# Optimization experiments

Measured on AMD Instinct MI355X. Metric: run time of the kernel, lower is better.

The kernel has to match this reference:

```python
import jax, jax.numpy as jnp
import numpy as np
import math

EPS = 1e-6
KP = -1.0  # Poincare ball curvature (c=1 -> kappa=-1)
KS = 1.0   # stereographic sphere projection (c=1 -> kappa=+1)

def _n(x):
    return jnp.sqrt(jnp.sum(x * x, -1, keepdims=True) + 1e-15)

def tan_k(u, k):
    if k < 0:
        return jnp.tanh(u)
    return jnp.tan(jnp.clip(u, -1.47079, 1.47079))

def artan_k(u, k):
    if k < 0:
        return jnp.arctanh(jnp.clip(u, -1 + 1e-5, 1 - 1e-5))
    return jnp.arctan(u)

def proj(x, k):
    if k < 0:
        n = _n(x)
        m = 1.0 - 1e-4
        return jnp.where(n > m, x * (m / n), x)
    return x

def expmap0(u, k):
    n = _n(u)
    return proj(tan_k(n, k) * u / n, k)

def logmap0(y, k):
    n = _n(y)
    return artan_k(n, k) * y / n

def _safe_den(d):
    return jnp.where(d >= 0, jnp.maximum(d, EPS), jnp.minimum(d, -EPS))

def mobius_add(x, y, k):
    x2 = jnp.sum(x * x, -1, keepdims=True)
    y2 = jnp.sum(y * y, -1, keepdims=True)
    xy = jnp.sum(x * y, -1, keepdims=True)
    num = (1 - 2 * k * xy - k * y2) * x + (1 + k * x2) * y
    den = 1 - 2 * k * xy + k * k * x2 * y2
    return proj(num / _safe_den(den), k)

def mobius_pw_mul(w, x, k):
    wx = w * x
    nx = _n(x)
    nwx = _n(wx)
    return proj(tan_k(nwx / nx * artan_k(nx, k), k) * wx / nwx, k)

def mobius_smul(r, x, k):
    n = _n(x)
    return proj(tan_k(r * artan_k(n, k), k) * x / n, k)

def wmid(xs, k, axis, w=None):
    lam = 2.0 / (1.0 + k * jnp.sum(xs * xs, -1, keepdims=True))
    if w is None:
        w = jnp.ones_like(lam)
    num = jnp.sum(w * lam * xs, axis=axis)
    den = jnp.abs(jnp.sum(w * (lam - 1.0), axis=axis))
    return mobius_smul(0.5, num / jnp.maximum(den, EPS), k)

def slin(x, W, b, k=None):
    if k is None:
        return x @ W.T + b
    return expmap0(logmap0(x, k) @ W.T + b, k)

def dist(x, y, k):
    return 2.0 * artan_k(_n(mobius_add(-x, y, k))[..., 0], k)

def hyp_attn(kk, q, v, k):
    # kk, v: [N,K,h]; q: [N,h]
    sc = -dist(q[:, None, :], kk, k)              # [N,K]
    a = jax.nn.softmax(sc, axis=1)[..., None]
    return wmid(v, k, axis=1, w=a)

def euc_attn(kk, q, v):
    sc = jnp.einsum('nkh,nh->nk', kk, q) / math.sqrt(kk.shape[-1])
    a = jax.nn.softmax(sc, axis=1)
    return jnp.einsum('nk,nkh->nh', a, v)


def _forward(x, h1, c1, h2, c2, h3, c3, del_t, iou1, iou2, iou3,
             Wq_w, Wq_b, Wc_w, Wc_b, Uf_w, Uf_b, Up_w, Up_b,
             Uiou_w, Uiou_b, d, nbr):
    sg, th = jax.nn.sigmoid, jnp.tanh
    # mailbox gather (message_func + DGL mailbox), [N,K,h]
    mh1, mh2, mh3 = h1[nbr], h2[nbr], h3[nbr]
    mc1, mc2, mc3 = c1[nbr], c2[nbr], c3[nbr]
    g_t = (d / (del_t[nbr] + 1.0))[..., None]      # [N,K,1]

    x_1p = slin(expmap0(x, KP), Wq_w, Wq_b, KP)
    x_1s = slin(expmap0(x, KS), Wq_w, Wq_b, KS)
    x_1e = slin(x, Wq_w, Wq_b)

    s1 = logmap0(sg(slin(mh1, Up_w, Up_b, KP)), KP)
    s2 = logmap0(sg(slin(mh2, Up_w, Up_b, KS)), KS)
    s3 = sg(slin(mh3, Up_w, Up_b))

    ht1p = mobius_pw_mul(s1, mh1, KP)
    ht2p = mobius_pw_mul(s2, expmap0(logmap0(mh2, KS), KP), KP)
    ht3p = mobius_pw_mul(s3, expmap0(mh3, KP), KP)
    h_1p = 3.0 * wmid(jnp.stack([ht1p, ht2p, ht3p]), KP, axis=0)

    ht1s = mobius_pw_mul(s1, expmap0(logmap0(mh1, KP), KS), KP)
    ht2s = mobius_pw_mul(s2, mh2, KS)
    ht3s = mobius_pw_mul(s3, expmap0(mh3, KS), KS)
    h_1s = 3.0 * wmid(jnp.stack([ht1s, ht2s, ht3s]), KP, axis=0)

    ht1e = logmap0(mobius_pw_mul(s1, mh1, KP), KP)
    ht2e = logmap0(mobius_pw_mul(s2, mh2, KS), KS)
    h_1e = ht1e + ht2e + s3 * mh3

    h_tildp = hyp_attn(h_1p, x_1p, h_1p, KP)
    h_tilds = hyp_attn(h_1s, x_1s, h_1s, KS)
    h_tilde = euc_attn(h_1e, x_1e, h_1e)

    # Poincare cell path
    csk_p = expmap0(th(logmap0(slin(mc1, Wc_w, Wc_b, KP), KP)), KP)
    ckt_p = mobius_add(mobius_add(-csk_p, mc1, KP), mobius_pw_mul(csk_p, g_t, KP), KP)
    f_p = sg(logmap0(slin(mh1, Uf_w, Uf_b, KP), KP))
    c_1 = wmid(mobius_pw_mul(f_p, ckt_p, KP), KP, axis=1)

    # Sphere cell path
    csk_s = expmap0(th(logmap0(slin(mc2, Wc_w, Wc_b, KS), KS)), KS)
    ckt_s = mobius_add(mobius_add(-csk_s, mc2, KS), mobius_pw_mul(csk_s, g_t, KS), KS)
    f_s = sg(logmap0(slin(mh2, Uf_w, Uf_b, KS), KS))
    c_2 = wmid(mobius_pw_mul(f_s, ckt_s, KS), KS, axis=1)

    # Euclidean cell path
    csk_e = th(slin(mc3, Wc_w, Wc_b))
    ckt_e = mc3 - csk_e + csk_e * g_t
    f_e = sg(slin(mh3, Uf_w, Uf_b))
    c_3 = jnp.sum(f_e * ckt_e, 1)

    niou1 = mobius_add(iou1, slin(h_tildp, Uiou_w, Uiou_b, KP), KP)
    niou2 = mobius_add(iou2, slin(h_tilds, Uiou_w, Uiou_b, KS), KS)
    niou3 = iou3 + slin(h_tilde, Uiou_w, Uiou_b)

    # apply_node_func
    i_p, o_p, u_p = jnp.split(niou1, 3, axis=1)
    i_p, o_p, u_p = sg(logmap0(i_p, KP)), sg(logmap0(o_p, KP)), th(logmap0(u_p, KP))
    i_s, o_s, u_s = jnp.split(niou2, 3, axis=1)
    i_s, o_s, u_s = sg(logmap0(i_s, KS)), sg(logmap0(o_s, KS)), th(logmap0(u_s, KS))
    i_e, o_e, u_e = jnp.split(niou3, 3, axis=1)
    i_e, o_e, u_e = sg(i_e), sg(o_e), th(u_e)

    nc1 = mobius_add(mobius_pw_mul(i_p, u_p, KP), c_1, KP)
    nc2 = mobius_add(mobius_pw_mul(i_s, u_s, KS), c_2, KS)
    nc3 = i_e * u_e + c_3
    nh1 = mobius_pw_mul(o_p, th(logmap0(nc1, KP)), KP)
    nh2 = mobius_pw_mul(o_s, th(logmap0(nc2, KS)), KS)
    nh3 = o_e * th(nc3)
    return jnp.stack([nh1, nc1, nh2, nc2, nh3, nc3])  # [6,N,h]


def setup_inputs() -> dict:
    N, K, H, X = 8192, 8, 128, 128
    key = jax.random.key(0)
    ks = jax.random.split(key, 24)
    def rn(i, shape, sc=0.05):
        return sc * jax.random.normal(ks[i], shape, jnp.float32)
    return dict(
        x=rn(0, (N, X)), h1=rn(1, (N, H)), c1=rn(2, (N, H)),
        h2=rn(3, (N, H)), c2=rn(4, (N, H)), h3=rn(5, (N, H)), c3=rn(6, (N, H)),
        del_t=jax.random.uniform(ks[7], (N,), jnp.float32),
        iou1=rn(8, (N, 3 * H)), iou2=rn(9, (N, 3 * H)), iou3=rn(10, (N, 3 * H)),
        Wq_w=rn(11, (H, X)), Wq_b=rn(12, (H,), 0.01),
        Wc_w=rn(13, (H, H)), Wc_b=rn(14, (H,), 0.01),
        Uf_w=rn(15, (H, H)), Uf_b=rn(16, (H,), 0.01),
        Up_w=rn(17, (H, H)), Up_b=rn(18, (H,), 0.01),
        Uiou_w=rn(19, (3 * H, H)), Uiou_b=rn(20, (3 * H,), 0.01),
        d=jnp.asarray(60.0, jnp.float32),
        nbr=jax.random.randint(ks[21], (N, K), 0, N),
    )


def reference(x, h1, c1, h2, c2, h3, c3, del_t, iou1, iou2, iou3,
              Wq_w, Wq_b, Wc_w, Wc_b, Uf_w, Uf_b, Up_w, Up_b,
              Uiou_w, Uiou_b, d, nbr):
    return _forward(x, h1, c1, h2, c2, h3, c3, del_t, iou1, iou2, iou3,
                    Wq_w, Wq_b, Wc_w, Wc_b, Uf_w, Uf_b, Up_w, Up_b,
                    Uiou_w, Uiou_b, d, nbr)
```

## Files before the change

kernel.cpp:

```cpp
#include <hip/hip_runtime.h>
#include <math.h>

#define HD 128
#define NNODE 8192
#define KNBR 8
#define NHS ((size_t)NNODE*(size_t)HD)

#define EPSF 1e-6f
#define PMX 0.9999f
#define ATHC (1.0f-1e-5f)
#define TANC 1.47079f

typedef unsigned short u16;
typedef unsigned int u32;
typedef __attribute__((ext_vector_type(8))) short short8;
typedef __attribute__((ext_vector_type(4))) float f32x4;
typedef __attribute__((ext_vector_type(2))) float f32x2;

static __device__ __forceinline__ float frcp(float x){ return __builtin_amdgcn_rcpf(x); }
static __device__ __forceinline__ float fdiv(float a,float b){ return a*__builtin_amdgcn_rcpf(b); }
static __device__ __forceinline__ float fsqrt(float x){ return __builtin_amdgcn_sqrtf(x); }
static __device__ __forceinline__ float fexp(float x){ return __builtin_amdgcn_exp2f(x*1.4426950408889634f); }
static __device__ __forceinline__ float flog(float x){ return __builtin_amdgcn_logf(x)*0.6931471805599453f; }
static __device__ __forceinline__ float ftanh(float x){
  float ax = fabsf(x);
  float e = fexp(-2.0f*ax);
  float t = (1.0f-e)*frcp(1.0f+e);
  return copysignf(t,x);
}
static __device__ __forceinline__ float fatanh(float x){
  x = fminf(fmaxf(x,-ATHC),ATHC);
  return 0.5f*flog((1.0f+x)*frcp(1.0f-x));
}
static __device__ __forceinline__ float fatan(float x){
  float ax = fabsf(x);
  bool inv = ax > 1.0f;
  float t = inv ? frcp(ax) : ax;
  float t2 = t*t;
  float p = -0.0117212f;
  p = p*t2 + 0.05265332f;
  p = p*t2 - 0.11643287f;
  p = p*t2 + 0.19354346f;
  p = p*t2 - 0.33262347f;
  p = p*t2 + 0.99997726f;
  float r = t*p;
  r = inv ? 1.5707963267948966f - r : r;
  return copysignf(r,x);
}
static __device__ __forceinline__ float ftan(float x){
  x = fminf(fmaxf(x,-TANC),TANC);
  float r = x*0.15915494309189535f;
  float s = __builtin_amdgcn_sinf(r);
  float c = __builtin_amdgcn_cosf(r);
  return s*frcp(c);
}
static __device__ __forceinline__ float sigm(float x){ return frcp(1.0f+fexp(-x)); }
static __device__ __forceinline__ float safeden(float d){
  return d>=0.0f ? fmaxf(d,EPSF) : fminf(d,-EPSF);
}

static __device__ __forceinline__ float wred(float v){
#pragma unroll
  for(int m=32;m;m>>=1) v += __shfl_xor(v,m,64);
  return v;
}
static __device__ __forceinline__ float hred16(float v){
#pragma unroll
  for(int m=8;m;m>>=1) v += __shfl_xor(v,m,64);
  return v;
}

static __device__ __forceinline__ u16 f2bf(float f){
  u32 u = __float_as_uint(f);
  u32 r = u + 0x7fffu + ((u>>16)&1u);
  return (u16)(r>>16);
}
static __device__ __forceinline__ float bf2f(u16 h){
  return __uint_as_float(((u32)h)<<16);
}
static __device__ __forceinline__ void split2(float v, u16* hp, u16* lp){
  u16 h = f2bf(v);
  float r = v - bf2f(h);
  *hp = h; *lp = f2bf(r);
}
static __device__ __forceinline__ void split2x2(float v0, float v1, u16* hp, u16* lp){
  u16 h0 = f2bf(v0), h1 = f2bf(v1);
  float r0 = v0 - bf2f(h0), r1 = v1 - bf2f(h1);
  *(u32*)hp = (u32)h0 | ((u32)h1<<16);
  *(u32*)lp = (u32)f2bf(r0) | ((u32)f2bf(r1)<<16);
}

#define SCOFF (27*NHS)
#define WOFF  (27*NHS + 49152)
#define NW    114688

__global__ __launch_bounds__(256) void k_pre(
    const float* __restrict__ x, const float* __restrict__ h1,
    const float* __restrict__ h2, const float* __restrict__ c1,
    const float* __restrict__ c2, const float* __restrict__ h3,
    const float* __restrict__ c3,
    const float* __restrict__ Wq, const float* __restrict__ Wc,
    const float* __restrict__ Uf, const float* __restrict__ Up,
    const float* __restrict__ Uiou, float* __restrict__ ws)
{
  if(blockIdx.x >= 2048){
    u16* WH = (u16*)(ws + WOFF);
    u16* WL = WH + NW;
    int idx0 = ((blockIdx.x-2048)*256 + threadIdx.x)*4;
#pragma unroll
    for(int q=0;q<4;q+=2){
      int idx = idx0 + q;
      float v0, v1;
      if(idx < 16384)      { v0=Wq[idx]; v1=Wq[idx+1]; }
      else if(idx < 32768) { v0=Wc[idx-16384]; v1=Wc[idx-16383]; }
      else if(idx < 49152) { v0=Uf[idx-32768]; v1=Uf[idx-32767]; }
      else if(idx < 65536) { v0=Up[idx-49152]; v1=Up[idx-49151]; }
      else                 { v0=Uiou[idx-65536]; v1=Uiou[idx-65535]; }
      split2x2(v0, v1, &WH[idx], &WL[idx]);
    }
    return;
  }
  int row = blockIdx.x*4 + (threadIdx.x>>6);
  int l = threadIdx.x & 63;
  size_t i0 = (size_t)row*HD + 2*l;
#define LD2(p) (*(const f32x2*)&p[i0])
  f32x2 xv = LD2(x);
  f32x2 h1v = LD2(h1), h2v = LD2(h2), h3v = LD2(h3);
  f32x2 c1v = LD2(c1), c2v = LD2(c2), c3v = LD2(c3);
#undef LD2
  float xa=xv[0], xb=xv[1];
  float h1a=h1v[0], h1b=h1v[1];
  float h2a=h2v[0], h2b=h2v[1];
  float c1a=c1v[0], c1b=c1v[1];
  float c2a=c2v[0], c2b=c2v[1];
  float h3a=h3v[0], h3b=h3v[1];
  float c3a=c3v[0], c3b=c3v[1];
  float xsq = wred(xa*xa+xb*xb);
  float h1sq = wred(h1a*h1a+h1b*h1b);
  float h2sq = wred(h2a*h2a+h2b*h2b);
  float c1sq = wred(c1a*c1a+c1b*c1b);
  float c2sq = wred(c2a*c2a+c2b*c2b);
  size_t p0 = i0;
#define WRSPLIT(R, va, vb) { \
    u16* hp = (u16*)(ws + (size_t)(R)*NHS); u16* lp2 = hp + NHS; \
    split2x2(va, vb, &hp[p0], &lp2[p0]); }
  float nx = fsqrt(xsq+1e-15f);
  {
    float t = ftanh(nx);
    float f = fminf(t,PMX)*frcp(nx);
    float ny = fsqrt(f*f*xsq + 1e-15f);
    float g = fatanh(ny)*frcp(ny) * f;
    WRSPLIT(0, g*xa, g*xb)
  }
  {
    float t = ftan(nx);
    float f = t*frcp(nx);
    float ny = fsqrt(f*f*xsq + 1e-15f);
    float g = fatan(ny)*frcp(ny) * f;
    WRSPLIT(1, g*xa, g*xb)
  }
  WRSPLIT(2, xa, xb)
  { float n=fsqrt(h1sq+1e-15f); float g=fatanh(n)*frcp(n); WRSPLIT(3, g*h1a, g*h1b) }
  { float n=fsqrt(h2sq+1e-15f); float g=fatan(n)*frcp(n);  WRSPLIT(4, g*h2a, g*h2b) }
  WRSPLIT(5, h3a, h3b)
  { float n=fsqrt(c1sq+1e-15f); float g=fatanh(n)*frcp(n); WRSPLIT(6, g*c1a, g*c1b) }
  { float n=fsqrt(c2sq+1e-15f); float g=fatan(n)*frcp(n);  WRSPLIT(7, g*c2a, g*c2b) }
  WRSPLIT(8, c3a, c3b)
#undef WRSPLIT
}

enum { P_ID=0, P_EXP_P, P_EXP_S, P_SIG, P_TANH, P_SIG_LOG_P, P_SIG_LOG_S,
       P_LOGSIG_P, P_LOGSIG_S, P_TANH_EXP_P, P_TANH_EXP_S };

struct JobM { const u16* Ah; const u16* Al; const u16* Wh; const u16* Wl;
              const float* b; float* out; int pitch; int post; };
struct JobTabM { JobM j[12]; };

__global__ __launch_bounds__(512) void k_gemmM(JobTabM tab){
  JobM jb = tab.j[blockIdx.y];
  __shared__ u16 Wlds[2*8*4*64*8];
  const int tid = threadIdx.x;
  for(int c = tid; c < 4096; c += 512){
    int lane_ = c & 63;
    int kk    = (c>>6)&3;
    int t     = (c>>8)&7;
    int plane = (c>>11)&1;
    const u16* src = (plane ? jb.Wl : jb.Wh)
                   + (size_t)(t*16 + (lane_&15))*128 + (lane_>>4)*8 + kk*32;
    *(uint4*)&Wlds[(size_t)c*8] = *(const uint4*)src;
  }
  const int lane = tid & 63;
  const int wave = tid >> 6;
  const int nn = lane & 15, quad = lane >> 4;
  float bias[8];
#pragma unroll
  for(int t=0;t<8;t++) bias[t] = jb.b[t*16+nn];
  __syncthreads();
  {
    const int row0 = blockIdx.x*128 + wave*16;
    const u16* Ah = jb.Ah + (size_t)(row0+nn)*128 + quad*8;
    const u16* Al = jb.Al + (size_t)(row0+nn)*128 + quad*8;
    f32x4 acc[8];
#pragma unroll
    for(int t=0;t<8;t++) acc[t] = (f32x4){0.f,0.f,0.f,0.f};
#pragma unroll
    for(int kk=0;kk<4;kk++){
      short8 ah = *(const short8*)(Ah + kk*32);
      short8 al = *(const short8*)(Al + kk*32);
#pragma unroll
      for(int t=0;t<8;t++){
        short8 wh = *(const short8*)&Wlds[(((0*8 + t)*4 + kk)*64 + lane)*8];
        short8 wl = *(const short8*)&Wlds[(((1*8 + t)*4 + kk)*64 + lane)*8];
        acc[t] = __builtin_amdgcn_mfma_f32_16x16x32_bf16(ah, wh, acc[t], 0,0,0);
        acc[t] = __builtin_amdgcn_mfma_f32_16x16x32_bf16(al, wh, acc[t], 0,0,0);
        acc[t] = __builtin_amdgcn_mfma_f32_16x16x32_bf16(ah, wl, acc[t], 0,0,0);
      }
    }
#pragma unroll
    for(int r=0;r<4;r++){
      float v[8];
#pragma unroll
      for(int t=0;t<8;t++) v[t] = acc[t][r] + bias[t];
      float s2 = 0.f;
#pragma unroll
      for(int t=0;t<8;t++) s2 += v[t]*v[t];
      float nraw = hred16(s2);
      switch(jb.post){
        case P_ID: break;
        case P_EXP_P: {
          float n=fsqrt(nraw+1e-15f); float tt=ftanh(n); float f=fminf(tt,PMX)*frcp(n);
          for(int t=0;t<8;t++) v[t]*=f;
        } break;
        case P_EXP_S: {
          float n=fsqrt(nraw+1e-15f); float f=ftan(n)*frcp(n);
          for(int t=0;t<8;t++) v[t]*=f;
        } break;
        case P_SIG:
          for(int t=0;t<8;t++) v[t]=sigm(v[t]);
          break;
        case P_TANH:
          for(int t=0;t<8;t++) v[t]=ftanh(v[t]);
          break;
        case P_SIG_LOG_P: {
          float n=fsqrt(nraw+1e-15f); float tt=ftanh(n); float f=fminf(tt,PMX)*frcp(n);
          float z[8]; float zs=0.f;
          for(int t=0;t<8;t++){ z[t]=sigm(f*v[t]); zs+=z[t]*z[t]; }
          float zr=hred16(zs);
          float zn=fsqrt(zr+1e-15f);
          float g=fatanh(zn)*frcp(zn);
          for(int t=0;t<8;t++) v[t]=g*z[t];
        } break;
        case P_SIG_LOG_S: {
          float n=fsqrt(nraw+1e-15f); float f=ftan(n)*frcp(n);
          float z[8]; float zs=0.f;
          for(int t=0;t<8;t++){ z[t]=sigm(f*v[t]); zs+=z[t]*z[t]; }
          float zr=hred16(zs);
          float zn=fsqrt(zr+1e-15f);
          float g=fatan(zn)*frcp(zn);
          for(int t=0;t<8;t++) v[t]=g*z[t];
        } break;
        case P_LOGSIG_P: {
          float n=fsqrt(nraw+1e-15f); float tt=ftanh(n); float f=fminf(tt,PMX)*frcp(n);
          float ny=fsqrt(f*f*nraw+1e-15f);
          float g=fatanh(ny)*frcp(ny)*f;
          for(int t=0;t<8;t++) v[t]=sigm(g*v[t]);
        } break;
        case P_LOGSIG_S: {
          float n=fsqrt(nraw+1e-15f); float f=ftan(n)*frcp(n);
          float ny=fsqrt(f*f*nraw+1e-15f);
          float g=fatan(ny)*frcp(ny)*f;
          for(int t=0;t<8;t++) v[t]=sigm(g*v[t]);
        } break;
        case P_TANH_EXP_P: {
          float n=fsqrt(nraw+1e-15f); float tt=ftanh(n); float f=fminf(tt,PMX)*frcp(n);
          float ny=fsqrt(f*f*nraw+1e-15f);
          float g=fatanh(ny)*frcp(ny)*f;
          float T[8]; float Ts=0.f;
          for(int t=0;t<8;t++){ T[t]=ftanh(g*v[t]); Ts+=T[t]*T[t]; }
          float Tr=hred16(Ts);
          float Tn=fsqrt(Tr+1e-15f);
          float t2=ftanh(Tn); float f2=fminf(t2,PMX)*frcp(Tn);
          for(int t=0;t<8;t++) v[t]=f2*T[t];
        } break;
        case P_TANH_EXP_S: {
          float n=fsqrt(nraw+1e-15f); float f=ftan(n)*frcp(n);
          float ny=fsqrt(f*f*nraw+1e-15f);
          float g=fatan(ny)*frcp(ny)*f;
          float T[8]; float Ts=0.f;
          for(int t=0;t<8;t++){ T[t]=ftanh(g*v[t]); Ts+=T[t]*T[t]; }
          float Tr=hred16(Ts);
          float Tn=fsqrt(Tr+1e-15f);
          float f2=ftan(Tn)*frcp(Tn);
          for(int t=0;t<8;t++) v[t]=f2*T[t];
        } break;
      }
      float* orow = jb.out + (size_t)(row0 + quad*4 + r)*jb.pitch + nn;
#pragma unroll
      for(int t=0;t<8;t++) orow[t*16] = v[t];
    }
  }
}

__global__ __launch_bounds__(256) void k_phaseB(
  const float* __restrict__ h1,const float* __restrict__ h2,const float* __restrict__ h3,
  const float* __restrict__ c1,const float* __restrict__ c2,const float* __restrict__ c3,
  const float* __restrict__ del_t, const float* __restrict__ dsc,
  float* __restrict__ ws)
{
  const float* S1 = ws+9*NHS;  const float* S2 = ws+10*NHS; const float* S3 = ws+11*NHS;
  const float* F1 = ws+12*NHS; const float* F2 = ws+13*NHS; const float* F3 = ws+14*NHS;
  const float* Q1 = ws+15*NHS; const float* Q2 = ws+16*NHS; const float* Q3 = ws+17*NHS;
  f32x2* PKP = (f32x2*)(ws+21*NHS);
  f32x2* PKS = (f32x2*)(ws+22*NHS);
  f32x2* PKE = (f32x2*)(ws+23*NHS);
  f32x4* PKV4= (f32x4*)(ws+24*NHS);
  f32x2* PKV2= (f32x2*)(ws+26*NHS);
  f32x4* SC4 = (f32x4*)(ws+SCOFF);

  int j = blockIdx.x*4 + (threadIdx.x>>6);
  int l = threadIdx.x&63;
  size_t i0 = (size_t)j*HD + 2*l;
  size_t pix = (size_t)j*64 + l;
#define LD2(p) (*(const f32x2*)&p[i0])
  f32x2 h1v=LD2(h1), h2v=LD2(h2), h3v=LD2(h3);
  f32x2 c1v=LD2(c1), c2v=LD2(c2), c3v=LD2(c3);
  f32x2 s1v=LD2(S1), s2v=LD2(S2), s3v=LD2(S3);
  f32x2 f1v=LD2(F1), f2v=LD2(F2), f3v=LD2(F3);
  f32x2 q1v=LD2(Q1), q2v=LD2(Q2), q3v=LD2(Q3);
#undef LD2
  float h1a=h1v[0],h1b=h1v[1], h2a=h2v[0],h2b=h2v[1], h3a=h3v[0],h3b=h3v[1];
  float c1a=c1v[0],c1b=c1v[1], c2a=c2v[0],c2b=c2v[1], c3a=c3v[0],c3b=c3v[1];
  float s1a=s1v[0],s1b=s1v[1], s2a=s2v[0],s2b=s2v[1], s3a=s3v[0],s3b=s3v[1];
  float f1a=f1v[0],f1b=f1v[1], f2a=f2v[0],f2b=f2v[1], f3a=f3v[0],f3b=f3v[1];
  float q1a=q1v[0],q1b=q1v[1], q2a=q2v[0],q2b=q2v[1], q3a=q3v[0],q3b=q3v[1];
  float g = fdiv(dsc[0], del_t[j]+1.0f);

  float h1sq = wred(h1a*h1a+h1b*h1b); float n1 = fsqrt(h1sq+1e-15f);
  float h2sq = wred(h2a*h2a+h2b*h2b); float n2 = fsqrt(h2sq+1e-15f);
  float h3sq = wred(h3a*h3a+h3b*h3b); float n3 = fsqrt(h3sq+1e-15f);
  float w1a=s1a*h1a, w1b=s1b*h1b;
  float w2a=s2a*h2a, w2b=s2b*h2b;
  float w3a=s3a*h3a, w3b=s3b*h3b;
  float w1sq = wred(w1a*w1a+w1b*w1b); float nw1 = fsqrt(w1sq+1e-15f);
  float w2sq = wred(w2a*w2a+w2b*w2b); float nw2 = fsqrt(w2sq+1e-15f);
  float w3sq = wred(w3a*w3a+w3b*w3b); float nw3 = fsqrt(w3sq+1e-15f);

  float t1 = ftanh(nw1*frcp(n1) * fatanh(n1));
  float fp1 = fminf(t1,PMX)*frcp(nw1); float np1 = fminf(t1,PMX);
  float nu2 = fatan(n2);
  float ne2 = fminf(ftanh(nu2),PMX);
  float t2 = ftanh(nw2*frcp(n2) * fatanh(ne2));
  float fp2 = fminf(t2,PMX)*frcp(nw2); float np2 = fminf(t2,PMX);
  float ne3 = fminf(ftanh(n3),PMX);
  float t3 = ftanh(nw3*frcp(n3) * fatanh(ne3));
  float fp3 = fminf(t3,PMX)*frcp(nw3); float np3 = fminf(t3,PMX);
  float y2pv;
  {
    float lamA = 2.0f*frcp(1.0f-np1*np1), lamB = 2.0f*frcp(1.0f-np2*np2), lamC = 2.0f*frcp(1.0f-np3*np3);
    float dn = frcp(fmaxf(fabsf(lamA+lamB+lamC-3.0f), EPSF));
    float va = (lamA*fp1*w1a + lamB*fp2*w2a + lamC*fp3*w3a)*dn;
    float vb = (lamA*fp1*w1b + lamB*fp2*w2b + lamC*fp3*w3b)*dn;
    float vsq = wred(va*va+vb*vb); float nv = fsqrt(vsq+1e-15f);
    float tt = ftanh(0.5f*fatanh(nv)); float ff = 3.0f*fminf(tt,PMX)*frcp(nv);
    PKP[pix] = (f32x2){ff*va, ff*vb};
    y2pv = ff*ff*vsq;
  }
  float t2s, fs2, y2sv;
  {
    float nx1s = ftan(fatanh(n1));
    float t1s = ftanh(nw1*frcp(n1) * fatanh(nx1s));
    float fs1 = fminf(t1s,PMX)*frcp(nw1); float ns1 = fminf(t1s,PMX);
    t2s = ftan(nw2*frcp(n2) * fatan(n2));
    fs2 = t2s*frcp(nw2);
    float nx3s = ftan(n3);
    float t3s = ftan(nw3*frcp(n3) * fatan(nx3s));
    float fs3 = t3s*frcp(nw3);
    float lA = 2.0f*frcp(1.0f-ns1*ns1), lB = 2.0f*frcp(1.0f-t2s*t2s), lC = 2.0f*frcp(1.0f-t3s*t3s);
    float dns = frcp(fmaxf(fabsf(lA+lB+lC-3.0f), EPSF));
    float vsa = (lA*fs1*w1a + lB*fs2*w2a + lC*fs3*w3a)*dns;
    float vsb = (lA*fs1*w1b + lB*fs2*w2b + lC*fs3*w3b)*dns;
    float vssq = wred(vsa*vsa+vsb*vsb); float nvs = fsqrt(vssq+1e-15f);
    float tts = ftan(0.5f*fatan(nvs)); float ffs = 3.0f*tts*frcp(nvs);
    PKS[pix] = (f32x2){ffs*vsa, ffs*vsb};
    y2sv = ffs*ffs*vssq;
  }
  {
    float ne1 = fsqrt(fp1*fp1*w1sq + 1e-15f);
    float ge1 = fatanh(ne1)*frcp(ne1);
    float n2s_ = fsqrt(fs2*fs2*w2sq + 1e-15f);
    float ge2 = fatan(n2s_)*frcp(n2s_);
    float h1ea = ge1*fp1*w1a + ge2*fs2*w2a + s3a*h3a;
    float h1eb = ge1*fp1*w1b + ge2*fs2*w2b + s3b*h3b;
    PKE[pix] = (f32x2){h1ea, h1eb};
  }
  float ng = fsqrt(g*g+1e-15f);
  float v1xa,v1xb,d1v;
  {
    float q1sq = wred(q1a*q1a+q1b*q1b);
    float c1rs = wred(c1a*c1a+c1b*c1b);
    float dq1 = wred(q1a*c1a+q1b*c1b);
    float xy = -dq1;
    float aa = 1.0f+2.0f*xy+c1rs, bb = 1.0f-q1sq;
    float dd = frcp(safeden(1.0f+2.0f*xy+q1sq*c1rs));
    float m1a = (aa*(-q1a)+bb*c1a)*dd, m1b = (aa*(-q1b)+bb*c1b)*dd;
    float m1sq = (aa*aa*q1sq + 2.0f*aa*bb*xy + bb*bb*c1rs)*dd*dd;
    float mdq = (-aa*q1sq + bb*dq1)*dd;
    { float nm = fsqrt(m1sq+1e-15f);
      if(nm>PMX){ float sc=PMX*frcp(nm); m1a*=sc; m1b*=sc; m1sq*=sc*sc; mdq*=sc; } }
    float nwg = fsqrt(g*g*q1sq+1e-15f);
    float tg = ftanh(nwg*frcp(ng) * fatanh(ng));
    float fX = fminf(tg,PMX)*frcp(nwg) * g;
    float X2sq = fX*fX*q1sq;
    float xy2 = fX*mdq;
    float a2 = 1.0f+2.0f*xy2+X2sq, b2 = 1.0f-m1sq;
    float d2d = frcp(safeden(1.0f+2.0f*xy2+m1sq*X2sq));
    float ka = (a2*m1a + b2*fX*q1a)*d2d, kb = (a2*m1b + b2*fX*q1b)*d2d;
    float ksq = (a2*a2*m1sq + 2.0f*a2*b2*xy2 + b2*b2*X2sq)*d2d*d2d;
    { float nk0 = fsqrt(ksq+1e-15f);
      if(nk0>PMX){ float sc=PMX*frcp(nk0); ka*=sc; kb*=sc; ksq*=sc*sc; } }
    float nk = fsqrt(ksq+1e-15f);
    float wfa = f1a*ka, wfb = f1b*kb;
    float wfsq = wred(wfa*wfa+wfb*wfb); float nwf = fsqrt(wfsq+1e-15f);
    float tu = ftanh(nwf*frcp(nk) * fatanh(nk));
    float fu = fminf(tu,PMX)*frcp(nwf);
    float u1sq = fu*fu*wfsq;
    float lam = 2.0f*frcp(1.0f-u1sq);
    v1xa=lam*fu*wfa; v1xb=lam*fu*wfb;
    d1v=lam-1.0f;
  }
  float v2xa,v2xb,d2v;
  {
    float q2sq = wred(q2a*q2a+q2b*q2b);
    float c2rs = wred(c2a*c2a+c2b*c2b);
    float dq2 = wred(q2a*c2a+q2b*c2b);
    float xy = -dq2;
    float aa = 1.0f-2.0f*xy-c2rs, bb = 1.0f+q2sq;
    float dd = frcp(safeden(1.0f-2.0f*xy+q2sq*c2rs));
    float ma = (aa*(-q2a)+bb*c2a)*dd, mb = (aa*(-q2b)+bb*c2b)*dd;
    float msq = (aa*aa*q2sq + 2.0f*aa*bb*xy + bb*bb*c2rs)*dd*dd;
    float mdq = (-aa*q2sq + bb*dq2)*dd;
    float nwg = fsqrt(g*g*q2sq+1e-15f);
    float tg = ftan(nwg*frcp(ng) * fatan(ng));
    float fX = tg*frcp(nwg) * g;
    float X2sq = fX*fX*q2sq;
    float xy2 = fX*mdq;
    float a2 = 1.0f-2.0f*xy2-X2sq, b2 = 1.0f+msq;
    float d2d = frcp(safeden(1.0f-2.0f*xy2+msq*X2sq));
    float ka = (a2*ma + b2*fX*q2a)*d2d, kb = (a2*mb + b2*fX*q2b)*d2d;
    float ksq = (a2*a2*msq + 2.0f*a2*b2*xy2 + b2*b2*X2sq)*d2d*d2d;
    float nk = fsqrt(ksq+1e-15f);
    float wfa = f2a*ka, wfb = f2b*kb;
    float wfsq = wred(wfa*wfa+wfb*wfb); float nwf = fsqrt(wfsq+1e-15f);
    float tu = ftan(nwf*frcp(nk) * fatan(nk));
    float fu = tu*frcp(nwf);
    float u2sq = fu*fu*wfsq;
    float lam = 2.0f*frcp(1.0f+u2sq);
    v2xa=lam*fu*wfa; v2xb=lam*fu*wfb;
    d2v=lam-1.0f;
  }
  float v3xa,v3xb;
  {
    float kea = c3a + q3a*(g-1.0f), keb = c3b + q3b*(g-1.0f);
    v3xa=f3a*kea; v3xb=f3b*keb;
  }
  PKV4[pix] = (f32x4){v1xa,v1xb,v2xa,v2xb};
  PKV2[pix] = (f32x2){v3xa,v3xb};
  if(l==0) SC4[j] = (f32x4){y2pv,y2sv,d1v,d2v};
}

__global__ __launch_bounds__(256) void k_attn(
  const int* __restrict__ nbr, float* __restrict__ ws)
{
  const f32x2* PKP = (const f32x2*)(ws+21*NHS);
  const f32x2* PKS = (const f32x2*)(ws+22*NHS);
  const f32x2* PKE = (const f32x2*)(ws+23*NHS);
  const f32x4* PKV4= (const f32x4*)(ws+24*NHS);
  const f32x2* PKV2= (const f32x2*)(ws+26*NHS);
  const float* SCf = ws+SCOFF;
  u16* LPh = (u16*)(ws+9*NHS);  u16* LPl = LPh + NHS;
  u16* LSh = (u16*)(ws+10*NHS); u16* LSl = LSh + NHS;
  u16* LEh = (u16*)(ws+11*NHS); u16* LEl = LEh + NHS;
  float* C1o = ws+12*NHS; float* C2o = ws+13*NHS; float* C3o = ws+14*NHS;
  float* c1n2 = ws+SCOFF+32768; float* c2n2 = ws+SCOFF+40960;

  int n = blockIdx.x;
  int wv = threadIdx.x>>6;
  int l = threadIdx.x&63;
  size_t i0 = (size_t)n*HD + 2*l;
  int4 jA = ((const int4*)nbr)[n*2+0];
  int4 jB = ((const int4*)nbr)[n*2+1];
  int js[8] = {jA.x,jA.y,jA.z,jA.w,jB.x,jB.y,jB.z,jB.w};

  if(wv==0){
    const float* XP = ws+18*NHS;
    f32x2 xv = *(const f32x2*)&XP[i0];
    float XPa=xv[0], XPb=xv[1];
    float x2p = wred(XPa*XPa+XPb*XPb);
    float Ha[8],Hb[8],y2k[8];
#pragma unroll
    for(int k=0;k<8;k++){
      int j = js[k];
      f32x2 h = PKP[(size_t)j*64+l];
      Ha[k]=h[0]; Hb[k]=h[1];
      y2k[k]=SCf[(size_t)j*4+0];
    }
    float sc[8];
#pragma unroll
    for(int k=0;k<8;k++){
      float dp = wred(XPa*Ha[k]+XPb*Hb[k]);
      float xy=-dp, y2=y2k[k];
      float aa=1.0f+2.0f*xy+y2, bb=1.0f-x2p;
      float dd=frcp(safeden(1.0f+2.0f*xy+x2p*y2));
      float nsq=(aa*aa*x2p+2.0f*aa*bb*xy+bb*bb*y2)*dd*dd;
      float nn=fminf(fsqrt(nsq+1e-15f),PMX);
      sc[k] = -2.0f*fatanh(nn);
    }
    float mx=sc[0];
#pragma unroll
    for(int k=1;k<8;k++) mx=fmaxf(mx,sc[k]);
    float a[8]; float s=0;
#pragma unroll
    for(int k=0;k<8;k++){ a[k]=fexp(sc[k]-mx); s+=a[k]; }
    float inv=frcp(s);
    float na=0,nb=0,de=0;
#pragma unroll
    for(int k=0;k<8;k++){
      float lam = 2.0f*frcp(1.0f-y2k[k]); float w=a[k]*inv;
      na+=w*lam*Ha[k]; nb+=w*lam*Hb[k]; de+=w*(lam-1.0f);
    }
    de = frcp(fmaxf(fabsf(de),EPSF));
    na*=de; nb*=de;
    float vsq=wred(na*na+nb*nb); float nv=fsqrt(vsq+1e-15f);
    float tt=ftanh(0.5f*fatanh(nv)); float f=fminf(tt,PMX)*frcp(nv);
    float ha=f*na, hb=f*nb;
    float hn=fsqrt(f*f*vsq+1e-15f);
    float gl=fatanh(hn)*frcp(hn);
    split2x2(gl*ha, gl*hb, &LPh[i0], &LPl[i0]);
  } else if(wv==1){
    const float* XS = ws+19*NHS;
    f32x2 xv = *(const f32x2*)&XS[i0];
    float XSa=xv[0], XSb=xv[1];
    float x2s = wred(XSa*XSa+XSb*XSb);
    float Ha[8],Hb[8],y2k[8];
#pragma unroll
    for(int k=0;k<8;k++){
      int j = js[k];
      f32x2 h = PKS[(size_t)j*64+l];
      Ha[k]=h[0]; Hb[k]=h[1];
      y2k[k]=SCf[(size_t)j*4+1];
    }
    float sc[8];
#pragma unroll
    for(int k=0;k<8;k++){
      float dsv = wred(XSa*Ha[k]+XSb*Hb[k]);
      float xy=-dsv, y2=y2k[k];
      float aa=1.0f-2.0f*xy-y2, bb=1.0f+x2s;
      float dd=frcp(safeden(1.0f-2.0f*xy+x2s*y2));
      float nsq=(aa*aa*x2s+2.0f*aa*bb*xy+bb*bb*y2)*dd*dd;
      float nn=fsqrt(nsq+1e-15f);
      sc[k] = -2.0f*fatan(nn);
    }
    float mx=sc[0];
#pragma unroll
    for(int k=1;k<8;k++) mx=fmaxf(mx,sc[k]);
    float a[8]; float s=0;
#pragma unroll
    for(int k=0;k<8;k++){ a[k]=fexp(sc[k]-mx); s+=a[k]; }
    float inv=frcp(s);
    float na=0,nb=0,de=0;
#pragma unroll
    for(int k=0;k<8;k++){
      float lam = 2.0f*frcp(1.0f+y2k[k]); float w=a[k]*inv;
      na+=w*lam*Ha[k]; nb+=w*lam*Hb[k]; de+=w*(lam-1.0f);
    }
    de = frcp(fmaxf(fabsf(de),EPSF));
    na*=de; nb*=de;
    float vsq=wred(na*na+nb*nb); float nv=fsqrt(vsq+1e-15f);
    float tt=ftan(0.5f*fatan(nv)); float f=tt*frcp(nv);
    float ha=f*na, hb=f*nb;
    float hn=fsqrt(f*f*vsq+1e-15f);
    float gl=fatan(hn)*frcp(hn);
    split2x2(gl*ha, gl*hb, &LSh[i0], &LSl[i0]);
  } else if(wv==2){
    const float* XE = ws+20*NHS;
    const float rs = 0.08838834764831845f;
    f32x2 xv = *(const f32x2*)&XE[i0];
    float XEa=xv[0], XEb=xv[1];
    float Ha[8],Hb[8];
#pragma unroll
    for(int k=0;k<8;k++){
      int j = js[k];
      f32x2 h = PKE[(size_t)j*64+l];
      Ha[k]=h[0]; Hb[k]=h[1];
    }
    float sc[8];
#pragma unroll
    for(int k=0;k<8;k++) sc[k] = wred(XEa*Ha[k]+XEb*Hb[k])*rs;
    float mx=sc[0];
#pragma unroll
    for(int k=1;k<8;k++) mx=fmaxf(mx,sc[k]);
    float a[8]; float s=0;
#pragma unroll
    for(int k=0;k<8;k++){ a[k]=fexp(sc[k]-mx); s+=a[k]; }
    float inv=frcp(s);
    float ha=0,hb=0;
#pragma unroll
    for(int k=0;k<8;k++){ float w=a[k]*inv; ha+=w*Ha[k]; hb+=w*Hb[k]; }
    split2x2(ha, hb, &LEh[i0], &LEl[i0]);
  } else {
    float v1a=0,v1b=0,v2a=0,v2b=0,v3a=0,v3b=0,ds1=0,ds2=0;
#pragma unroll
    for(int k=0;k<8;k++){
      int j = js[k];
      f32x4 v4 = PKV4[(size_t)j*64+l];
      f32x2 v2 = PKV2[(size_t)j*64+l];
      v1a+=v4[0]; v1b+=v4[1]; v2a+=v4[2]; v2b+=v4[3];
      v3a+=v2[0]; v3b+=v2[1];
      ds1+=SCf[(size_t)j*4+2]; ds2+=SCf[(size_t)j*4+3];
    }
    {
      float de=frcp(fmaxf(fabsf(ds1),EPSF));
      float na=v1a*de, nb=v1b*de;
      float vsq=wred(na*na+nb*nb); float nv=fsqrt(vsq+1e-15f);
      float tt=ftanh(0.5f*fatanh(nv)); float f=fminf(tt,PMX)*frcp(nv);
      *(f32x2*)&C1o[i0] = (f32x2){f*na, f*nb};
      if(l==0) c1n2[n]=f*f*vsq;
    }
    {
      float de=frcp(fmaxf(fabsf(ds2),EPSF));
      float na=v2a*de, nb=v2b*de;
      float vsq=wred(na*na+nb*nb); float nv=fsqrt(vsq+1e-15f);
      float tt=ftan(0.5f*fatan(nv)); float f=tt*frcp(nv);
      *(f32x2*)&C2o[i0] = (f32x2){f*na, f*nb};
      if(l==0) c2n2[n]=f*f*vsq;
    }
    *(f32x2*)&C3o[i0] = (f32x2){v3a, v3b};
  }
}

__global__ __launch_bounds__(256) void k_final(
  const float* __restrict__ iou1, const float* __restrict__ iou2,
  const float* __restrict__ iou3, float* __restrict__ ws,
  float* __restrict__ out)
{
  const float* YP = ws; const float* YS = ws+3*NHS; const float* YE = ws+6*NHS;
  const float* C1v = ws+12*NHS; const float* C2v = ws+13*NHS; const float* C3v = ws+14*NHS;
  const float* c1n2 = ws+SCOFF+32768; const float* c2n2 = ws+SCOFF+40960;
  int n = blockIdx.x*4 + (threadIdx.x>>6);
  int l = threadIdx.x&63;
  size_t b384 = (size_t)n*384 + 2*l;
  size_t b128 = (size_t)n*HD + 2*l;
  {
    float Y[6], I[6];
#pragma unroll
    for(int p=0;p<3;p++){
      f32x2 yv = *(const f32x2*)&YP[b384 + 128*p];
      f32x2 iv = *(const f32x2*)&iou1[b384 + 128*p];
      Y[2*p]=yv[0]; Y[2*p+1]=yv[1]; I[2*p]=iv[0]; I[2*p+1]=iv[1];
    }
    float sy=0,si=0,sx=0;
#pragma unroll
    for(int r=0;r<6;r++){ sy+=Y[r]*Y[r]; si+=I[r]*I[r]; sx+=I[r]*Y[r]; }
    sy=wred(sy); si=wred(si); sx=wred(sx);
    float nY=fsqrt(sy+1e-15f);
    float te=ftanh(nY); float fE=fminf(te,PMX)*frcp(nY);
    float y2=fE*fE*sy, x2=si, xy=fE*sx;
    float aa=1.0f+2.0f*xy+y2, bb=1.0f-x2;
    float dd=frcp(safeden(1.0f+2.0f*xy+x2*y2));
    float nio[6];
#pragma unroll
    for(int r=0;r<6;r++) nio[r]=(aa*I[r]+bb*fE*Y[r])*dd;
    float nsq=(aa*aa*x2+2.0f*aa*bb*xy+bb*bb*y2)*dd*dd;
    { float nn=fsqrt(nsq+1e-15f);
      if(nn>PMX){ float sc=PMX*frcp(nn); for(int r=0;r<6;r++) nio[r]*=sc; } }
    float ci=wred(nio[0]*nio[0]+nio[1]*nio[1]); float ni=fsqrt(ci+1e-15f); float gi=fatanh(ni)*frcp(ni);
    float ip0=sigm(gi*nio[0]), ip1=sigm(gi*nio[1]);
    float co=wred(nio[2]*nio[2]+nio[3]*nio[3]); float no=fsqrt(co+1e-15f); float go=fatanh(no)*frcp(no);
    float op0=sigm(go*nio[2]), op1=sigm(go*nio[3]);
    float cu=wred(nio[4]*nio[4]+nio[5]*nio[5]); float nu=fsqrt(cu+1e-15f); float gu=fatanh(nu)*frcp(nu);
    float up0=ftanh(gu*nio[4]), up1=ftanh(gu*nio[5]);
    float usq=wred(up0*up0+up1*up1); float nx=fsqrt(usq+1e-15f);
    float wv0=ip0*up0, wv1=ip1*up1;
    float wsq=wred(wv0*wv0+wv1*wv1); float nwx=fsqrt(wsq+1e-15f);
    float tP=ftanh(nwx*frcp(nx)*fatanh(nx)); float fP=fminf(tP,PMX)*frcp(nwx);
    float P0=fP*wv0, P1=fP*wv1; float p2=fP*fP*wsq;
    f32x2 cv = *(const f32x2*)&C1v[b128];
    float ca=cv[0], cb=cv[1];
    float y2c=c1n2[n];
    float xyc=wred(P0*ca+P1*cb);
    float a3=1.0f+2.0f*xyc+y2c, b3=1.0f-p2;
    float d3=frcp(safeden(1.0f+2.0f*xyc+p2*y2c));
    float nc0=(a3*P0+b3*ca)*d3, nc1_=(a3*P1+b3*cb)*d3;
    float ncsq=(a3*a3*p2+2.0f*a3*b3*xyc+b3*b3*y2c)*d3*d3;
    { float nn=fsqrt(ncsq+1e-15f);
      if(nn>PMX){ float sc=PMX*frcp(nn); nc0*=sc; nc1_*=sc; ncsq*=sc*sc; } }
    float nl=fsqrt(ncsq+1e-15f);
    float gL=fatanh(nl)*frcp(nl);
    float T0=ftanh(gL*nc0), T1=ftanh(gL*nc1_);
    float tsq=wred(T0*T0+T1*T1); float nT=fsqrt(tsq+1e-15f);
    float wo0=op0*T0, wo1=op1*T1;
    float osq=wred(wo0*wo0+wo1*wo1); float nwo=fsqrt(osq+1e-15f);
    float tH=ftanh(nwo*frcp(nT)*fatanh(nT)); float fH=fminf(tH,PMX)*frcp(nwo);
    *(f32x2*)&out[0*NHS + b128] = (f32x2){fH*wo0, fH*wo1};
    *(f32x2*)&out[1*NHS + b128] = (f32x2){nc0, nc1_};
  }
  {
    float Y[6], I[6];
#pragma unroll
    for(int p=0;p<3;p++){
      f32x2 yv = *(const f32x2*)&YS[b384 + 128*p];
      f32x2 iv = *(const f32x2*)&iou2[b384 + 128*p];
      Y[2*p]=yv[0]; Y[2*p+1]=yv[1]; I[2*p]=iv[0]; I[2*p+1]=iv[1];
    }
    float sy=0,si=0,sx=0;
#pragma unroll
    for(int r=0;r<6;r++){ sy+=Y[r]*Y[r]; si+=I[r]*I[r]; sx+=I[r]*Y[r]; }
    sy=wred(sy); si=wred(si); sx=wred(sx);
    float nY=fsqrt(sy+1e-15f);
    float te=ftan(nY); float fE=te*frcp(nY);
    float y2=fE*fE*sy, x2=si, xy=fE*sx;
    float aa=1.0f-2.0f*xy-y2, bb=1.0f+x2;
    float dd=frcp(safeden(1.0f-2.0f*xy+x2*y2));
    float nio[6];
#pragma unroll
    for(int r=0;r<6;r++) nio[r]=(aa*I[r]+bb*fE*Y[r])*dd;
    float ci=wred(nio[0]*nio[0]+nio[1]*nio[1]); float ni=fsqrt(ci+1e-15f); float gi=fatan(ni)*frcp(ni);
    float ip0=sigm(gi*nio[0]), ip1=sigm(gi*nio[1]);
    float co=wred(nio[2]*nio[2]+nio[3]*nio[3]); float no=fsqrt(co+1e-15f); float go=fatan(no)*frcp(no);
    float op0=sigm(go*nio[2]), op1=sigm(go*nio[3]);
    float cu=wred(nio[4]*nio[4]+nio[5]*nio[5]); float nu=fsqrt(cu+1e-15f); float gu=fatan(nu)*frcp(nu);
    float up0=ftanh(gu*nio[4]), up1=ftanh(gu*nio[5]);
    float usq=wred(up0*up0+up1*up1); float nx=fsqrt(usq+1e-15f);
    float wv0=ip0*up0, wv1=ip1*up1;
    float wsq=wred(wv0*wv0+wv1*wv1); float nwx=fsqrt(wsq+1e-15f);
    float tP=ftan(nwx*frcp(nx)*fatan(nx)); float fP=tP*frcp(nwx);
    float P0=fP*wv0, P1=fP*wv1; float p2=fP*fP*wsq;
    f32x2 cv = *(const f32x2*)&C2v[b128];
    float ca=cv[0], cb=cv[1];
    float y2c=c2n2[n];
    float xyc=wred(P0*ca+P1*cb);
    float a3=1.0f-2.0f*xyc-y2c, b3=1.0f+p2;
    float d3=frcp(safeden(1.0f-2.0f*xyc+p2*y2c));
    float nc0=(a3*P0+b3*ca)*d3, nc1_=(a3*P1+b3*cb)*d3;
    float ncsq=(a3*a3*p2+2.0f*a3*b3*xyc+b3*b3*y2c)*d3*d3;
    float nl=fsqrt(ncsq+1e-15f);
    float gL=fatan(nl)*frcp(nl);
    float T0=ftanh(gL*nc0), T1=ftanh(gL*nc1_);
    float tsq=wred(T0*T0+T1*T1); float nT=fsqrt(tsq+1e-15f);
    float wo0=op0*T0, wo1=op1*T1;
    float osq=wred(wo0*wo0+wo1*wo1); float nwo=fsqrt(osq+1e-15f);
    float tH=ftan(nwo*frcp(nT)*fatan(nT)); float fH=tH*frcp(nwo);
    *(f32x2*)&out[2*NHS + b128] = (f32x2){fH*wo0, fH*wo1};
    *(f32x2*)&out[3*NHS + b128] = (f32x2){nc0, nc1_};
  }
  {
    float Y[6], I[6];
#pragma unroll
    for(int p=0;p<3;p++){
      f32x2 yv = *(const f32x2*)&YE[b384 + 128*p];
      f32x2 iv = *(const f32x2*)&iou3[b384 + 128*p];
      Y[2*p]=yv[0]; Y[2*p+1]=yv[1]; I[2*p]=iv[0]; I[2*p+1]=iv[1];
    }
    float n0=I[0]+Y[0], n1=I[1]+Y[1];
    float n2=I[2]+Y[2], n3=I[3]+Y[3];
    float n4=I[4]+Y[4], n5=I[5]+Y[5];
    float ie0=sigm(n0), ie1=sigm(n1);
    float oe0=sigm(n2), oe1=sigm(n3);
    float ue0=ftanh(n4), ue1=ftanh(n5);
    f32x2 cv = *(const f32x2*)&C3v[b128];
    float ca=cv[0], cb=cv[1];
    float nc0=ie0*ue0+ca, nc1_=ie1*ue1+cb;
    *(f32x2*)&out[4*NHS + b128] = (f32x2){oe0*ftanh(nc0), oe1*ftanh(nc1_)};
    *(f32x2*)&out[5*NHS + b128] = (f32x2){nc0, nc1_};
  }
}

extern "C" void kernel_launch(void* const* d_in, const int* in_sizes, int n_in,
                              void* d_out, int out_size, void* d_ws, size_t ws_size,
                              hipStream_t stream)
{
  const float* x     = (const float*)d_in[0];
  const float* h1    = (const float*)d_in[1];
  const float* c1    = (const float*)d_in[2];
  const float* h2    = (const float*)d_in[3];
  const float* c2    = (const float*)d_in[4];
  const float* h3    = (const float*)d_in[5];
  const float* c3    = (const float*)d_in[6];
  const float* del_t = (const float*)d_in[7];
  const float* iou1  = (const float*)d_in[8];
  const float* iou2  = (const float*)d_in[9];
  const float* iou3  = (const float*)d_in[10];
  const float* Wq_w  = (const float*)d_in[11];
  const float* Wq_b  = (const float*)d_in[12];
  const float* Wc_w  = (const float*)d_in[13];
  const float* Wc_b  = (const float*)d_in[14];
  const float* Uf_w  = (const float*)d_in[15];
  const float* Uf_b  = (const float*)d_in[16];
  const float* Up_w  = (const float*)d_in[17];
  const float* Up_b  = (const float*)d_in[18];
  const float* Uiou_w= (const float*)d_in[19];
  const float* Uiou_b= (const float*)d_in[20];
  const float* dsc   = (const float*)d_in[21];
  const int*   nbr   = (const int*)d_in[22];
  float* out = (float*)d_out;
  float* ws  = (float*)d_ws;

  k_pre<<<2160,256,0,stream>>>(x,h1,h2,c1,c2,h3,c3,Wq_w,Wc_w,Uf_w,Up_w,Uiou_w,ws);

  u16* WH = (u16*)(ws + WOFF);
  u16* WL = WH + NW;
  const u16* Wqh = WH;           const u16* Wql = WL;
  const u16* Wch = WH + 16384;   const u16* Wcl = WL + 16384;
  const u16* Ufh = WH + 32768;   const u16* Ufl = WL + 32768;
  const u16* Uph = WH + 49152;   const u16* Upl = WL + 49152;
  const u16* UIh = WH + 65536;   const u16* UIl = WL + 65536;
#define APLANE(R) ((const u16*)(ws + (size_t)(R)*NHS)), ((const u16*)(ws + (size_t)(R)*NHS) + NHS)

  JobTabM A{};
  A.j[0]  = { APLANE(0), Wqh, Wql, Wq_b, ws+18*NHS, 128, P_EXP_P };
  A.j[1]  = { APLANE(1), Wqh, Wql, Wq_b, ws+19*NHS, 128, P_EXP_S };
  A.j[2]  = { APLANE(2), Wqh, Wql, Wq_b, ws+20*NHS, 128, P_ID };
  A.j[3]  = { APLANE(3), Uph, Upl, Up_b, ws+9*NHS,  128, P_SIG_LOG_P };
  A.j[4]  = { APLANE(4), Uph, Upl, Up_b, ws+10*NHS, 128, P_SIG_LOG_S };
  A.j[5]  = { APLANE(5), Uph, Upl, Up_b, ws+11*NHS, 128, P_SIG };
  A.j[6]  = { APLANE(3), Ufh, Ufl, Uf_b, ws+12*NHS, 128, P_LOGSIG_P };
  A.j[7]  = { APLANE(4), Ufh, Ufl, Uf_b, ws+13*NHS, 128, P_LOGSIG_S };
  A.j[8]  = { APLANE(5), Ufh, Ufl, Uf_b, ws+14*NHS, 128, P_SIG };
  A.j[9]  = { APLANE(6), Wch, Wcl, Wc_b, ws+15*NHS, 128, P_TANH_EXP_P };
  A.j[10] = { APLANE(7), Wch, Wcl, Wc_b, ws+16*NHS, 128, P_TANH_EXP_S };
  A.j[11] = { APLANE(8), Wch, Wcl, Wc_b, ws+17*NHS, 128, P_TANH };
  k_gemmM<<<dim3(NNODE/128,12),512,0,stream>>>(A);

  k_phaseB<<<2048,256,0,stream>>>(h1,h2,h3,c1,c2,c3,del_t,dsc,ws);
  k_attn<<<8192,256,0,stream>>>(nbr,ws);

  JobTabM B{};
  for(int ct=0; ct<3; ct++){
    B.j[0*3+ct] = { APLANE(9),  UIh + ct*16384, UIl + ct*16384, Uiou_b + ct*128, ws+0*NHS + ct*128, 384, P_ID };
    B.j[1*3+ct] = { APLANE(10), UIh + ct*16384, UIl + ct*16384, Uiou_b + ct*128, ws+3*NHS + ct*128, 384, P_ID };
    B.j[2*3+ct] = { APLANE(11), UIh + ct*16384, UIl + ct*16384, Uiou_b + ct*128, ws+6*NHS + ct*128, 384, P_ID };
  }
  k_gemmM<<<dim3(NNODE/128,9),512,0,stream>>>(B);

  k_final<<<2048,256,0,stream>>>(iou1,iou2,iou3,ws,out);
}
```

Baseline: 258.5 us.

## Store intermediate workspace tensors in fp16 and prefetch GEMM A operands before LDS fill

All intermediate buffers passed between kernels (GEMM outputs, the packed neighbor keys and values in phaseB and attention, the attention outputs, and the second GEMM's iou outputs) are now stored as fp16 instead of fp32. Values are converted back to fp32 on load. This halves the memory traffic of the workspace reads and writes, including the random neighbor gathers in k_attn. The GEMM kernel also issues its A-operand global loads before the LDS weight fill, so those loads overlap the fill and the barrier. The cost is lower precision in the intermediates (about 11 mantissa bits), which may drift from the fp32-accurate reference.

```diff
diff --git a/kernel.cpp b/kernel.cpp
--- a/kernel.cpp
+++ b/kernel.cpp
@@ -13,9 +13,12 @@
 
 typedef unsigned short u16;
 typedef unsigned int u32;
+typedef _Float16 f16;
 typedef __attribute__((ext_vector_type(8))) short short8;
 typedef __attribute__((ext_vector_type(4))) float f32x4;
 typedef __attribute__((ext_vector_type(2))) float f32x2;
+typedef __attribute__((ext_vector_type(2))) _Float16 f16x2;
+typedef __attribute__((ext_vector_type(4))) _Float16 f16x4;
 
 static __device__ __forceinline__ float frcp(float x){ return __builtin_amdgcn_rcpf(x); }
 static __device__ __forceinline__ float fdiv(float a,float b){ return a*__builtin_amdgcn_rcpf(b); }
@@ -78,16 +81,19 @@
 static __device__ __forceinline__ float bf2f(u16 h){
   return __uint_as_float(((u32)h)<<16);
 }
-static __device__ __forceinline__ void split2(float v, u16* hp, u16* lp){
-  u16 h = f2bf(v);
-  float r = v - bf2f(h);
-  *hp = h; *lp = f2bf(r);
-}
 static __device__ __forceinline__ void split2x2(float v0, float v1, u16* hp, u16* lp){
   u16 h0 = f2bf(v0), h1 = f2bf(v1);
   float r0 = v0 - bf2f(h0), r1 = v1 - bf2f(h1);
   *(u32*)hp = (u32)h0 | ((u32)h1<<16);
   *(u32*)lp = (u32)f2bf(r0) | ((u32)f2bf(r1)<<16);
+}
+
+static __device__ __forceinline__ f32x2 ldh2(const u16* p){
+  f16x2 v = *(const f16x2*)p;
+  return (f32x2){(float)v[0], (float)v[1]};
+}
+static __device__ __forceinline__ void sth2(u16* p, float a, float b){
+  *(f16x2*)p = (f16x2){(f16)a, (f16)b};
 }
 
 #define SCOFF (27*NHS)
@@ -173,13 +179,25 @@
        P_LOGSIG_P, P_LOGSIG_S, P_TANH_EXP_P, P_TANH_EXP_S };
 
 struct JobM { const u16* Ah; const u16* Al; const u16* Wh; const u16* Wl;
-              const float* b; float* out; int pitch; int post; };
+              const float* b; u16* out; int pitch; int post; };
 struct JobTabM { JobM j[12]; };
 
 __global__ __launch_bounds__(512) void k_gemmM(JobTabM tab){
   JobM jb = tab.j[blockIdx.y];
   __shared__ u16 Wlds[2*8*4*64*8];
   const int tid = threadIdx.x;
+  const int lane = tid & 63;
+  const int wave = tid >> 6;
+  const int nn = lane & 15, quad = lane >> 4;
+  const int row0 = blockIdx.x*128 + wave*16;
+  const u16* Ah = jb.Ah + (size_t)(row0+nn)*128 + quad*8;
+  const u16* Al = jb.Al + (size_t)(row0+nn)*128 + quad*8;
+  short8 ah[4], al[4];
+#pragma unroll
+  for(int kk=0;kk<4;kk++){
+    ah[kk] = *(const short8*)(Ah + kk*32);
+    al[kk] = *(const short8*)(Al + kk*32);
+  }
   for(int c = tid; c < 4096; c += 512){
     int lane_ = c & 63;
     int kk    = (c>>6)&3;
@@ -189,31 +207,23 @@
                    + (size_t)(t*16 + (lane_&15))*128 + (lane_>>4)*8 + kk*32;
     *(uint4*)&Wlds[(size_t)c*8] = *(const uint4*)src;
   }
-  const int lane = tid & 63;
-  const int wave = tid >> 6;
-  const int nn = lane & 15, quad = lane >> 4;
   float bias[8];
 #pragma unroll
   for(int t=0;t<8;t++) bias[t] = jb.b[t*16+nn];
   __syncthreads();
   {
-    const int row0 = blockIdx.x*128 + wave*16;
-    const u16* Ah = jb.Ah + (size_t)(row0+nn)*128 + quad*8;
-    const u16* Al = jb.Al + (size_t)(row0+nn)*128 + quad*8;
     f32x4 acc[8];
 #pragma unroll
     for(int t=0;t<8;t++) acc[t] = (f32x4){0.f,0.f,0.f,0.f};
 #pragma unroll
     for(int kk=0;kk<4;kk++){
-      short8 ah = *(const short8*)(Ah + kk*32);
-      short8 al = *(const short8*)(Al + kk*32);
 #pragma unroll
       for(int t=0;t<8;t++){
         short8 wh = *(const short8*)&Wlds[(((0*8 + t)*4 + kk)*64 + lane)*8];
         short8 wl = *(const short8*)&Wlds[(((1*8 + t)*4 + kk)*64 + lane)*8];
-        acc[t] = __builtin_amdgcn_mfma_f32_16x16x32_bf16(ah, wh, acc[t], 0,0,0);
-        acc[t] = __builtin_amdgcn_mfma_f32_16x16x32_bf16(al, wh, acc[t], 0,0,0);
-        acc[t] = __builtin_amdgcn_mfma_f32_16x16x32_bf16(ah, wl, acc[t], 0,0,0);
+        acc[t] = __builtin_amdgcn_mfma_f32_16x16x32_bf16(ah[kk], wh, acc[t], 0,0,0);
+        acc[t] = __builtin_amdgcn_mfma_f32_16x16x32_bf16(al[kk], wh, acc[t], 0,0,0);
+        acc[t] = __builtin_amdgcn_mfma_f32_16x16x32_bf16(ah[kk], wl, acc[t], 0,0,0);
       }
     }
 #pragma unroll
@@ -294,9 +304,9 @@
           for(int t=0;t<8;t++) v[t]=f2*T[t];
         } break;
       }
-      float* orow = jb.out + (size_t)(row0 + quad*4 + r)*jb.pitch + nn;
-#pragma unroll
-      for(int t=0;t<8;t++) orow[t*16] = v[t];
+      u16* orow = jb.out + (size_t)(row0 + quad*4 + r)*jb.pitch + nn;
+#pragma unroll
+      for(int t=0;t<8;t++) *(f16*)&orow[t*16] = (f16)v[t];
     }
   }
 }
@@ -307,14 +317,16 @@
   const float* __restrict__ del_t, const float* __restrict__ dsc,
   float* __restrict__ ws)
 {
-  const float* S1 = ws+9*NHS;  const float* S2 = ws+10*NHS; const float* S3 = ws+11*NHS;
-  const float* F1 = ws+12*NHS; const float* F2 = ws+13*NHS; const float* F3 = ws+14*NHS;
-  const float* Q1 = ws+15*NHS; const float* Q2 = ws+16*NHS; const float* Q3 = ws+17*NHS;
-  f32x2* PKP = (f32x2*)(ws+21*NHS);
-  f32x2* PKS = (f32x2*)(ws+22*NHS);
-  f32x2* PKE = (f32x2*)(ws+23*NHS);
-  f32x4* PKV4= (f32x4*)(ws+24*NHS);
-  f32x2* PKV2= (f32x2*)(ws+26*NHS);
+  const u16* S1 = (const u16*)(ws+9*NHS);  const u16* S2 = (const u16*)(ws+10*NHS);
+  const u16* S3 = (const u16*)(ws+11*NHS); const u16* F1 = (const u16*)(ws+12*NHS);
+  const u16* F2 = (const u16*)(ws+13*NHS); const u16* F3 = (const u16*)(ws+14*NHS);
+  const u16* Q1 = (const u16*)(ws+15*NHS); const u16* Q2 = (const u16*)(ws+16*NHS);
+  const u16* Q3 = (const u16*)(ws+17*NHS);
+  f16x2* PKP = (f16x2*)(ws+21*NHS);
+  f16x2* PKS = (f16x2*)(ws+22*NHS);
+  f16x2* PKE = (f16x2*)(ws+23*NHS);
+  f16x4* PKV4= (f16x4*)(ws+24*NHS);
+  f16x2* PKV2= (f16x2*)(ws+26*NHS);
   f32x4* SC4 = (f32x4*)(ws+SCOFF);
 
   int j = blockIdx.x*4 + (threadIdx.x>>6);
@@ -324,10 +336,10 @@
 #define LD2(p) (*(const f32x2*)&p[i0])
   f32x2 h1v=LD2(h1), h2v=LD2(h2), h3v=LD2(h3);
   f32x2 c1v=LD2(c1), c2v=LD2(c2), c3v=LD2(c3);
-  f32x2 s1v=LD2(S1), s2v=LD2(S2), s3v=LD2(S3);
-  f32x2 f1v=LD2(F1), f2v=LD2(F2), f3v=LD2(F3);
-  f32x2 q1v=LD2(Q1), q2v=LD2(Q2), q3v=LD2(Q3);
 #undef LD2
+  f32x2 s1v=ldh2(&S1[i0]), s2v=ldh2(&S2[i0]), s3v=ldh2(&S3[i0]);
+  f32x2 f1v=ldh2(&F1[i0]), f2v=ldh2(&F2[i0]), f3v=ldh2(&F3[i0]);
+  f32x2 q1v=ldh2(&Q1[i0]), q2v=ldh2(&Q2[i0]), q3v=ldh2(&Q3[i0]);
   float h1a=h1v[0],h1b=h1v[1], h2a=h2v[0],h2b=h2v[1], h3a=h3v[0],h3b=h3v[1];
   float c1a=c1v[0],c1b=c1v[1], c2a=c2v[0],c2b=c2v[1], c3a=c3v[0],c3b=c3v[1];
   float s1a=s1v[0],s1b=s1v[1], s2a=s2v[0],s2b=s2v[1], s3a=s3v[0],s3b=s3v[1];
@@ -362,7 +374,7 @@
     float vb = (lamA*fp1*w1b + lamB*fp2*w2b + lamC*fp3*w3b)*dn;
     float vsq = wred(va*va+vb*vb); float nv = fsqrt(vsq+1e-15f);
     float tt = ftanh(0.5f*fatanh(nv)); float ff = 3.0f*fminf(tt,PMX)*frcp(nv);
-    PKP[pix] = (f32x2){ff*va, ff*vb};
+    PKP[pix] = (f16x2){(f16)(ff*va), (f16)(ff*vb)};
     y2pv = ff*ff*vsq;
   }
   float t2s, fs2, y2sv;
@@ -381,7 +393,7 @@
     float vsb = (lA*fs1*w1b + lB*fs2*w2b + lC*fs3*w3b)*dns;
     float vssq = wred(vsa*vsa+vsb*vsb); float nvs = fsqrt(vssq+1e-15f);
     float tts = ftan(0.5f*fatan(nvs)); float ffs = 3.0f*tts*frcp(nvs);
-    PKS[pix] = (f32x2){ffs*vsa, ffs*vsb};
+    PKS[pix] = (f16x2){(f16)(ffs*vsa), (f16)(ffs*vsb)};
     y2sv = ffs*ffs*vssq;
   }
   {
@@ -391,7 +403,7 @@
     float ge2 = fatan(n2s_)*frcp(n2s_);
     float h1ea = ge1*fp1*w1a + ge2*fs2*w2a + s3a*h3a;
     float h1eb = ge1*fp1*w1b + ge2*fs2*w2b + s3b*h3b;
-    PKE[pix] = (f32x2){h1ea, h1eb};
+    PKE[pix] = (f16x2){(f16)h1ea, (f16)h1eb};
   }
   float ng = fsqrt(g*g+1e-15f);
   float v1xa,v1xb,d1v;
@@ -463,24 +475,24 @@
     float kea = c3a + q3a*(g-1.0f), keb = c3b + q3b*(g-1.0f);
     v3xa=f3a*kea; v3xb=f3b*keb;
   }
-  PKV4[pix] = (f32x4){v1xa,v1xb,v2xa,v2xb};
-  PKV2[pix] = (f32x2){v3xa,v3xb};
+  PKV4[pix] = (f16x4){(f16)v1xa,(f16)v1xb,(f16)v2xa,(f16)v2xb};
+  PKV2[pix] = (f16x2){(f16)v3xa,(f16)v3xb};
   if(l==0) SC4[j] = (f32x4){y2pv,y2sv,d1v,d2v};
 }
 
 __global__ __launch_bounds__(256) void k_attn(
   const int* __restrict__ nbr, float* __restrict__ ws)
 {
-  const f32x2* PKP = (const f32x2*)(ws+21*NHS);
-  const f32x2* PKS = (const f32x2*)(ws+22*NHS);
-  const f32x2* PKE = (const f32x2*)(ws+23*NHS);
-  const f32x4* PKV4= (const f32x4*)(ws+24*NHS);
-  const f32x2* PKV2= (const f32x2*)(ws+26*NHS);
+  const f16x2* PKP = (const f16x2*)(ws+21*NHS);
+  const f16x2* PKS = (const f16x2*)(ws+22*NHS);
+  const f16x2* PKE = (const f16x2*)(ws+23*NHS);
+  const f16x4* PKV4= (const f16x4*)(ws+24*NHS);
+  const f16x2* PKV2= (const f16x2*)(ws+26*NHS);
   const float* SCf = ws+SCOFF;
   u16* LPh = (u16*)(ws+9*NHS);  u16* LPl = LPh + NHS;
   u16* LSh = (u16*)(ws+10*NHS); u16* LSl = LSh + NHS;
   u16* LEh = (u16*)(ws+11*NHS); u16* LEl = LEh + NHS;
-  float* C1o = ws+12*NHS; float* C2o = ws+13*NHS; float* C3o = ws+14*NHS;
+  u16* C1o = (u16*)(ws+12*NHS); u16* C2o = (u16*)(ws+13*NHS); u16* C3o = (u16*)(ws+14*NHS);
   float* c1n2 = ws+SCOFF+32768; float* c2n2 = ws+SCOFF+40960;
 
   int n = blockIdx.x;
@@ -492,16 +504,16 @@
   int js[8] = {jA.x,jA.y,jA.z,jA.w,jB.x,jB.y,jB.z,jB.w};
 
   if(wv==0){
-    const float* XP = ws+18*NHS;
-    f32x2 xv = *(const f32x2*)&XP[i0];
+    const u16* XP = (const u16*)(ws+18*NHS);
+    f32x2 xv = ldh2(&XP[i0]);
     float XPa=xv[0], XPb=xv[1];
     float x2p = wred(XPa*XPa+XPb*XPb);
     float Ha[8],Hb[8],y2k[8];
 #pragma unroll
     for(int k=0;k<8;k++){
       int j = js[k];
-      f32x2 h = PKP[(size_t)j*64+l];
-      Ha[k]=h[0]; Hb[k]=h[1];
+      f16x2 h = PKP[(size_t)j*64+l];
+      Ha[k]=(float)h[0]; Hb[k]=(float)h[1];
       y2k[k]=SCf[(size_t)j*4+0];
     }
     float sc[8];
@@ -537,16 +549,16 @@
     float gl=fatanh(hn)*frcp(hn);
     split2x2(gl*ha, gl*hb, &LPh[i0], &LPl[i0]);
   } else if(wv==1){
-    const float* XS = ws+19*NHS;
-    f32x2 xv = *(const f32x2*)&XS[i0];
+    const u16* XS = (const u16*)(ws+19*NHS);
+    f32x2 xv = ldh2(&XS[i0]);
     float XSa=xv[0], XSb=xv[1];
     float x2s = wred(XSa*XSa+XSb*XSb);
     float Ha[8],Hb[8],y2k[8];
 #pragma unroll
     for(int k=0;k<8;k++){
       int j = js[k];
-      f32x2 h = PKS[(size_t)j*64+l];
-      Ha[k]=h[0]; Hb[k]=h[1];
+      f16x2 h = PKS[(size_t)j*64+l];
+      Ha[k]=(float)h[0]; Hb[k]=(float)h[1];
       y2k[k]=SCf[(size_t)j*4+1];
     }
     float sc[8];
@@ -582,16 +594,16 @@
     float gl=fatan(hn)*frcp(hn);
     split2x2(gl*ha, gl*hb, &LSh[i0], &LSl[i0]);
   } else if(wv==2){
-    const float* XE = ws+20*NHS;
+    const u16* XE = (const u16*)(ws+20*NHS);
     const float rs = 0.08838834764831845f;
-    f32x2 xv = *(const f32x2*)&XE[i0];
+    f32x2 xv = ldh2(&XE[i0]);
     float XEa=xv[0], XEb=xv[1];
     float Ha[8],Hb[8];
 #pragma unroll
     for(int k=0;k<8;k++){
       int j = js[k];
-      f32x2 h = PKE[(size_t)j*64+l];
-      Ha[k]=h[0]; Hb[k]=h[1];
+      f16x2 h = PKE[(size_t)j*64+l];
+      Ha[k]=(float)h[0]; Hb[k]=(float)h[1];
     }
     float sc[8];
 #pragma unroll
@@ -612,10 +624,10 @@
 #pragma unroll
     for(int k=0;k<8;k++){
       int j = js[k];
-      f32x4 v4 = PKV4[(size_t)j*64+l];
-      f32x2 v2 = PKV2[(size_t)j*64+l];
-      v1a+=v4[0]; v1b+=v4[1]; v2a+=v4[2]; v2b+=v4[3];
-      v3a+=v2[0]; v3b+=v2[1];
+      f16x4 v4 = PKV4[(size_t)j*64+l];
+      f16x2 v2 = PKV2[(size_t)j*64+l];
+      v1a+=(float)v4[0]; v1b+=(float)v4[1]; v2a+=(float)v4[2]; v2b+=(float)v4[3];
+      v3a+=(float)v2[0]; v3b+=(float)v2[1];
       ds1+=SCf[(size_t)j*4+2]; ds2+=SCf[(size_t)j*4+3];
     }
     {
@@ -623,7 +635,7 @@
       float na=v1a*de, nb=v1b*de;
       float vsq=wred(na*na+nb*nb); float nv=fsqrt(vsq+1e-15f);
       float tt=ftanh(0.5f*fatanh(nv)); float f=fminf(tt,PMX)*frcp(nv);
-      *(f32x2*)&C1o[i0] = (f32x2){f*na, f*nb};
+      sth2(&C1o[i0], f*na, f*nb);
       if(l==0) c1n2[n]=f*f*vsq;
     }
     {
@@ -631,10 +643,10 @@
       float na=v2a*de, nb=v2b*de;
       float vsq=wred(na*na+nb*nb); float nv=fsqrt(vsq+1e-15f);
       float tt=ftan(0.5f*fatan(nv)); float f=tt*frcp(nv);
-      *(f32x2*)&C2o[i0] = (f32x2){f*na, f*nb};
+      sth2(&C2o[i0], f*na, f*nb);
       if(l==0) c2n2[n]=f*f*vsq;
     }
-    *(f32x2*)&C3o[i0] = (f32x2){v3a, v3b};
+    sth2(&C3o[i0], v3a, v3b);
   }
 }
 
@@ -643,8 +655,12 @@
   const float* __restrict__ iou3, float* __restrict__ ws,
   float* __restrict__ out)
 {
-  const float* YP = ws; const float* YS = ws+3*NHS; const float* YE = ws+6*NHS;
-  const float* C1v = ws+12*NHS; const float* C2v = ws+13*NHS; const float* C3v = ws+14*NHS;
+  const u16* YP = (const u16*)ws;
+  const u16* YS = (const u16*)(ws+3*NHS);
+  const u16* YE = (const u16*)(ws+6*NHS);
+  const u16* C1v = (const u16*)(ws+12*NHS);
+  const u16* C2v = (const u16*)(ws+13*NHS);
+  const u16* C3v = (const u16*)(ws+14*NHS);
   const float* c1n2 = ws+SCOFF+32768; const float* c2n2 = ws+SCOFF+40960;
   int n = blockIdx.x*4 + (threadIdx.x>>6);
   int l = threadIdx.x&63;
@@ -654,7 +670,7 @@
     float Y[6], I[6];
 #pragma unroll
     for(int p=0;p<3;p++){
-      f32x2 yv = *(const f32x2*)&YP[b384 + 128*p];
+      f32x2 yv = ldh2(&YP[b384 + 128*p]);
       f32x2 iv = *(const f32x2*)&iou1[b384 + 128*p];
       Y[2*p]=yv[0]; Y[2*p+1]=yv[1]; I[2*p]=iv[0]; I[2*p+1]=iv[1];
     }
@@ -684,7 +700,7 @@
     float wsq=wred(wv0*wv0+wv1*wv1); float nwx=fsqrt(wsq+1e-15f);
     float tP=ftanh(nwx*frcp(nx)*fatanh(nx)); float fP=fminf(tP,PMX)*frcp(nwx);
     float P0=fP*wv0, P1=fP*wv1; float p2=fP*fP*wsq;
-    f32x2 cv = *(const f32x2*)&C1v[b128];
+    f32x2 cv = ldh2(&C1v[b128]);
     float ca=cv[0], cb=cv[1];
     float y2c=c1n2[n];
     float xyc=wred(P0*ca+P1*cb);
@@ -708,7 +724,7 @@
     float Y[6], I[6];
 #pragma unroll
     for(int p=0;p<3;p++){
-      f32x2 yv = *(const f32x2*)&YS[b384 + 128*p];
+      f32x2 yv = ldh2(&YS[b384 + 128*p]);
       f32x2 iv = *(const f32x2*)&iou2[b384 + 128*p];
       Y[2*p]=yv[0]; Y[2*p+1]=yv[1]; I[2*p]=iv[0]; I[2*p+1]=iv[1];
     }
@@ -735,7 +751,7 @@
     float wsq=wred(wv0*wv0+wv1*wv1); float nwx=fsqrt(wsq+1e-15f);
     float tP=ftan(nwx*frcp(nx)*fatan(nx)); float fP=tP*frcp(nwx);
     float P0=fP*wv0, P1=fP*wv1; float p2=fP*fP*wsq;
-    f32x2 cv = *(const f32x2*)&C2v[b128];
+    f32x2 cv = ldh2(&C2v[b128]);
     float ca=cv[0], cb=cv[1];
     float y2c=c2n2[n];
     float xyc=wred(P0*ca+P1*cb);
@@ -757,7 +773,7 @@
     float Y[6], I[6];
 #pragma unroll
     for(int p=0;p<3;p++){
-      f32x2 yv = *(const f32x2*)&YE[b384 + 128*p];
+      f32x2 yv = ldh2(&YE[b384 + 128*p]);
       f32x2 iv = *(const f32x2*)&iou3[b384 + 128*p];
       Y[2*p]=yv[0]; Y[2*p+1]=yv[1]; I[2*p]=iv[0]; I[2*p+1]=iv[1];
     }
@@ -767,7 +783,7 @@
     float ie0=sigm(n0), ie1=sigm(n1);
     float oe0=sigm(n2), oe1=sigm(n3);
     float ue0=ftanh(n4), ue1=ftanh(n5);
-    f32x2 cv = *(const f32x2*)&C3v[b128];
+    f32x2 cv = ldh2(&C3v[b128]);
     float ca=cv[0], cb=cv[1];
     float nc0=ie0*ue0+ca, nc1_=ie1*ue1+cb;
     *(f32x2*)&out[4*NHS + b128] = (f32x2){oe0*ftanh(nc0), oe1*ftanh(nc1_)};
@@ -817,18 +833,18 @@
 #define APLANE(R) ((const u16*)(ws + (size_t)(R)*NHS)), ((const u16*)(ws + (size_t)(R)*NHS) + NHS)
 
   JobTabM A{};
-  A.j[0]  = { APLANE(0), Wqh, Wql, Wq_b, ws+18*NHS, 128, P_EXP_P };
-  A.j[1]  = { APLANE(1), Wqh, Wql, Wq_b, ws+19*NHS, 128, P_EXP_S };
-  A.j[2]  = { APLANE(2), Wqh, Wql, Wq_b, ws+20*NHS, 128, P_ID };
-  A.j[3]  = { APLANE(3), Uph, Upl, Up_b, ws+9*NHS,  128, P_SIG_LOG_P };
-  A.j[4]  = { APLANE(4), Uph, Upl, Up_b, ws+10*NHS, 128, P_SIG_LOG_S };
-  A.j[5]  = { APLANE(5), Uph, Upl, Up_b, ws+11*NHS, 128, P_SIG };
-  A.j[6]  = { APLANE(3), Ufh, Ufl, Uf_b, ws+12*NHS, 128, P_LOGSIG_P };
-  A.j[7]  = { APLANE(4), Ufh, Ufl, Uf_b, ws+13*NHS, 128, P_LOGSIG_S };
-  A.j[8]  = { APLANE(5), Ufh, Ufl, Uf_b, ws+14*NHS, 128, P_SIG };
-  A.j[9]  = { APLANE(6), Wch, Wcl, Wc_b, ws+15*NHS, 128, P_TANH_EXP_P };
-  A.j[10] = { APLANE(7), Wch, Wcl, Wc_b, ws+16*NHS, 128, P_TANH_EXP_S };
-  A.j[11] = { APLANE(8), Wch, Wcl, Wc_b, ws+17*NHS, 128, P_TANH };
+  A.j[0]  = { APLANE(0), Wqh, Wql, Wq_b, (u16*)(ws+18*NHS), 128, P_EXP_P };
+  A.j[1]  = { APLANE(1), Wqh, Wql, Wq_b, (u16*)(ws+19*NHS), 128, P_EXP_S };
+  A.j[2]  = { APLANE(2), Wqh, Wql, Wq_b, (u16*)(ws+20*NHS), 128, P_ID };
+  A.j[3]  = { APLANE(3), Uph, Upl, Up_b, (u16*)(ws+9*NHS),  128, P_SIG_LOG_P };
+  A.j[4]  = { APLANE(4), Uph, Upl, Up_b, (u16*)(ws+10*NHS), 128, P_SIG_LOG_S };
+  A.j[5]  = { APLANE(5), Uph, Upl, Up_b, (u16*)(ws+11*NHS), 128, P_SIG };
+  A.j[6]  = { APLANE(3), Ufh, Ufl, Uf_b, (u16*)(ws+12*NHS), 128, P_LOGSIG_P };
+  A.j[7]  = { APLANE(4), Ufh, Ufl, Uf_b, (u16*)(ws+13*NHS), 128, P_LOGSIG_S };
+  A.j[8]  = { APLANE(5), Ufh, Ufl, Uf_b, (u16*)(ws+14*NHS), 128, P_SIG };
+  A.j[9]  = { APLANE(6), Wch, Wcl, Wc_b, (u16*)(ws+15*NHS), 128, P_TANH_EXP_P };
+  A.j[10] = { APLANE(7), Wch, Wcl, Wc_b, (u16*)(ws+16*NHS), 128, P_TANH_EXP_S };
+  A.j[11] = { APLANE(8), Wch, Wcl, Wc_b, (u16*)(ws+17*NHS), 128, P_TANH };
   k_gemmM<<<dim3(NNODE/128,12),512,0,stream>>>(A);
 
   k_phaseB<<<2048,256,0,stream>>>(h1,h2,h3,c1,c2,c3,del_t,dsc,ws);
@@ -836,9 +852,9 @@
 
   JobTabM B{};
   for(int ct=0; ct<3; ct++){
-    B.j[0*3+ct] = { APLANE(9),  UIh + ct*16384, UIl + ct*16384, Uiou_b + ct*128, ws+0*NHS + ct*128, 384, P_ID };
-    B.j[1*3+ct] = { APLANE(10), UIh + ct*16384, UIl + ct*16384, Uiou_b + ct*128, ws+3*NHS + ct*128, 384, P_ID };
-    B.j[2*3+ct] = { APLANE(11), UIh + ct*16384, UIl + ct*16384, Uiou_b + ct*128, ws+6*NHS + ct*128, 384, P_ID };
+    B.j[0*3+ct] = { APLANE(9),  UIh + ct*16384, UIl + ct*16384, Uiou_b + ct*128, (u16*)(ws+0*NHS) + ct*128, 384, P_ID };
+    B.j[1*3+ct] = { APLANE(10), UIh + ct*16384, UIl + ct*16384, Uiou_b + ct*128, (u16*)(ws+3*NHS) + ct*128, 384, P_ID };
+    B.j[2*3+ct] = { APLANE(11), UIh + ct*16384, UIl + ct*16384, Uiou_b + ct*128, (u16*)(ws+6*NHS) + ct*128, 384, P_ID };
   }
   k_gemmM<<<dim3(NNODE/128,9),512,0,stream>>>(B);
 
```

Measured after the change: 250.5 us. 3.1% less time.
